# Kernel optimization log

Hardware: AMD Instinct MI355X
Metric: run time of the kernel (lower is better)

The kernel has to match this reference:

```python
import math
import jax, jax.numpy as jnp
import numpy as np

D, N, B, L = 1024, 16, 8, 4096
SCALE = math.sqrt(1.0 / float(N))


def setup_inputs() -> dict:
    key = jax.random.key(0)
    ks = jax.random.split(key, 8)
    x = jax.random.normal(ks[0], (B, D, L), dtype=jnp.float32)
    p_logit = 0.2 * jax.random.normal(ks[1], (D, N), dtype=jnp.float32)
    # reset_parameters(): radius = 1 - sigmoid(p_logit) * delta, phases evenly spaced
    delta = jax.nn.sigmoid(0.2 * jax.random.normal(ks[2], (D, N), dtype=jnp.float32))
    freqs = jnp.exp(jnp.arange(1, D + 1, dtype=jnp.float32) * (-math.log(D) / float(D)))
    freqs = jax.random.permutation(ks[3], freqs)[:, None]            # (D,1)
    theta = freqs * (2.0 * math.pi / float(N))
    phi = theta * jnp.arange(1, N + 1, dtype=jnp.float32)[None, :]   # (D,N)
    p = jax.nn.sigmoid(p_logit)
    radius = 1.0 - p * delta                                         # in (0,1)
    log_q_real = jnp.log(radius)
    log_q_imag = phi
    gamma_real = jax.random.normal(ks[4], (D, N), dtype=jnp.float32)
    gamma_imag = jnp.zeros((D, N), dtype=jnp.float32)
    omega = 0.25 * jax.random.truncated_normal(ks[5], -4.0, 4.0, (D,), dtype=jnp.float32)
    return {"x": x, "p_logit": p_logit, "log_q_real": log_q_real,
            "log_q_imag": log_q_imag, "gamma_real": gamma_real,
            "gamma_imag": gamma_imag, "omega": omega}


def reference(x, p_logit, log_q_real, log_q_imag, gamma_real, gamma_imag, omega):
    # FFT path (hx=None, compute_last_state=False)
    p = jax.nn.sigmoid(p_logit).astype(jnp.float32)                  # (D,N)
    log_q = jax.lax.complex(log_q_real, log_q_imag)                  # complex64 (D,N)
    gamma = jax.lax.complex(gamma_real, gamma_imag) * SCALE          # (D,N)
    t = jnp.arange(L, dtype=jnp.float32)
    # q^t = exp(t * log_q)  (== cumprod of q in the torch code)
    q_pows = jnp.exp(log_q[:, :, None] * t[None, None, :])           # (D,N,L) complex64
    kernel = jnp.einsum('dn,dnl->dl', gamma * p.astype(gamma.dtype), q_pows)  # (D,L)
    fft_len = 1 << int(2 * L - 1).bit_length()
    X = jnp.fft.fft(x.astype(jnp.complex64), n=fft_len, axis=-1)     # (B,D,F)
    K = jnp.fft.fft(kernel, n=fft_len, axis=-1)                      # (D,F)
    y = jnp.fft.ifft(X * K[None], axis=-1)[..., :L].real.astype(x.dtype)
    residual = x * omega[None, :, None]
    return y + residual
```

## Files before the change

kernel.cpp:

```cpp
#include <hip/hip_runtime.h>
#include <hip/hip_bf16.h>
#include <math.h>

#define D_DIM   1024
#define NM      16
#define B_DIM   8
#define L_DIM   4096
#define SCALE_F 0.25f
#define NK      5
#define NITER   8
#define SROW    8704

typedef __attribute__((ext_vector_type(8))) short bf16x8;
typedef __attribute__((ext_vector_type(4))) float f32x4;

union U4 { uint4 u; bf16x8 v; };

__device__ __forceinline__ unsigned short f2bf(float f) {
    __hip_bfloat16 h = __float2bfloat16(f);
    return *reinterpret_cast<unsigned short*>(&h);
}
__device__ __forceinline__ float bflo(unsigned u) { return __uint_as_float(u << 16); }
__device__ __forceinline__ float bfhi(unsigned u) { return __uint_as_float(u & 0xffff0000u); }
__device__ __forceinline__ int swz(int a) { return a ^ (((a >> 7) & 7) << 4); }

__device__ void compute_af_k(int d, int lane, int k,
                             const float* __restrict__ p_logit,
                             const float* __restrict__ lqr,
                             const float* __restrict__ lqi,
                             const float* __restrict__ gr,
                             const float* __restrict__ gi,
                             char* __restrict__ afb)
{
    const int i = lane & 15, g = lane >> 4;
    const int t0 = i - 15 + 32 * k + 8 * g;
    const float t0f = (float)t0;

    float acc[8];
#pragma unroll
    for (int e = 0; e < 8; ++e) acc[e] = 0.0f;

#pragma unroll 1
    for (int n = 0; n < NM; ++n) {
        const int idx = d * NM + n;
        const float pp = 1.0f / (1.0f + __expf(-p_logit[idx]));
        const float CR = gr[idx] * (SCALE_F * pp);
        const float CI = gi[idx] * (SCALE_F * pp);
        const float LR = lqr[idx], LI = lqi[idx];

        float sq, cq; __sincosf(LI, &sq, &cq);
        const float eq = __expf(LR);
        const float qr = eq * cq, qi = eq * sq;
        float s0, c0; __sincosf(t0f * LI, &s0, &c0);
        const float e0 = __expf(t0f * LR);
        float wr = e0 * c0, wi = e0 * s0;

#pragma unroll
        for (int e = 0; e < 8; ++e) {
            acc[e] = fmaf(CR, wr, fmaf(-CI, wi, acc[e]));
            const float nwr = fmaf(wr, qr, -wi * qi);
            const float nwi = fmaf(wr, qi,  wi * qr);
            wr = nwr; wi = nwi;
        }
    }

    unsigned pk[4];
#pragma unroll
    for (int e = 0; e < 8; ++e) {
        const unsigned b = (t0 + e >= 0) ? (unsigned)f2bf(acc[e]) : 0u;
        if ((e & 1) == 0) pk[e >> 1] = b; else pk[e >> 1] |= b << 16;
    }
    *reinterpret_cast<uint4*>(afb + k * 1024 + lane * 16) =
        make_uint4(pk[0], pk[1], pk[2], pk[3]);
}

__global__ __launch_bounds__(512)
void ema_fused(const float* __restrict__ x,
               const float* __restrict__ p_logit,
               const float* __restrict__ lqr, const float* __restrict__ lqi,
               const float* __restrict__ gr, const float* __restrict__ gi,
               const float* __restrict__ omega,
               float* __restrict__ out)
{
    __shared__ __align__(16) char sstage[2][SROW];
    char* safb = sstage[1];

    const int tid  = threadIdx.x;
    const int w    = tid >> 6;
    const int lane = tid & 63;
    const int d    = blockIdx.x;
    const int j    = lane & 15, g = lane >> 4;

    const size_t rstride = (size_t)D_DIM * L_DIM;
    const float* xrow0 = x   + (size_t)d * L_DIM;
    float*       yrow0 = out + (size_t)d * L_DIM;
    const float  om    = omega[d];

    if (tid < 64) {
        const int buf = tid >> 5, h = tid & 31;
        *reinterpret_cast<uint4*>(sstage[buf] + swz(8192 + h * 16)) =
            make_uint4(0u, 0u, 0u, 0u);
    }

    float4 r[2];
#pragma unroll
    for (int v = 0; v < 2; ++v)
        r[v] = *reinterpret_cast<const float4*>(xrow0 + tid * 8 + 4 * v);

    if (w < NK)
        compute_af_k(d, lane, w, p_logit, lqr, lqi, gr, gi, safb);

    __syncthreads();

    bf16x8 af[NK];
#pragma unroll
    for (int k = 0; k < NK; ++k) {
        U4 u; u.u = *reinterpret_cast<const uint4*>(safb + k * 1024 + lane * 16);
        af[k] = u.v;
    }

#define PACK(dst)                                                              \
    {                                                                          \
        unsigned pk0 = (unsigned)f2bf(r[1].w) | ((unsigned)f2bf(r[1].z) << 16);\
        unsigned pk1 = (unsigned)f2bf(r[1].y) | ((unsigned)f2bf(r[1].x) << 16);\
        unsigned pk2 = (unsigned)f2bf(r[0].w) | ((unsigned)f2bf(r[0].z) << 16);\
        unsigned pk3 = (unsigned)f2bf(r[0].y) | ((unsigned)f2bf(r[0].x) << 16);\
        *reinterpret_cast<uint4*>((dst) + swz(8176 - tid * 16)) =              \
            make_uint4(pk0, pk1, pk2, pk3);                                    \
    }

    PACK(sstage[0]);
#pragma unroll
    for (int v = 0; v < 2; ++v)
        r[v] = *reinterpret_cast<const float4*>(xrow0 + rstride + tid * 8 + 4 * v);

    __syncthreads();

#pragma unroll 1
    for (int i = 0; i < NITER; ++i) {
        if (i < NITER - 1) {
            PACK(sstage[(i + 1) & 1]);
            if (i < NITER - 2) {
#pragma unroll
                for (int v = 0; v < 2; ++v)
                    r[v] = *reinterpret_cast<const float4*>(
                        xrow0 + (size_t)(i + 2) * rstride + tid * 8 + 4 * v);
            }
        }

        const char* sb = sstage[i & 1];
        float* yb = yrow0 + (size_t)i * rstride;
#pragma unroll
        for (int tt = 0; tt < 2; ++tt) {
            const int T = 2 * w + tt;
            f32x4 acc = {0.0f, 0.0f, 0.0f, 0.0f};
#pragma unroll
            for (int k = 0; k < NK; ++k) {
                const int rboff = 8160 - 512 * T - 32 * j + 64 * k + 16 * g;
                U4 z; z.u = *reinterpret_cast<const uint4*>(sb + swz(rboff));
                acc = __builtin_amdgcn_mfma_f32_16x16x32_bf16(af[k], z.v, acc, 0, 0, 0);
            }
            const int roff = 8184 - 512 * T - 32 * j - 8 * g;
            const uint2 z2 = *reinterpret_cast<const uint2*>(sb + swz(roff));
            acc.x = fmaf(om, bfhi(z2.y), acc.x);
            acc.y = fmaf(om, bflo(z2.y), acc.y);
            acc.z = fmaf(om, bfhi(z2.x), acc.z);
            acc.w = fmaf(om, bflo(z2.x), acc.w);
            __builtin_nontemporal_store(acc,
                reinterpret_cast<f32x4*>(yb + T * 256 + 16 * j + 4 * g));
        }

        if (i < NITER - 1)
            __syncthreads();
    }
#undef PACK
}

extern "C" void kernel_launch(void* const* d_in, const int* in_sizes, int n_in,
                              void* d_out, int out_size, void* d_ws, size_t ws_size,
                              hipStream_t stream)
{
    const float* x   = (const float*)d_in[0];
    const float* pl  = (const float*)d_in[1];
    const float* lqr = (const float*)d_in[2];
    const float* lqi = (const float*)d_in[3];
    const float* gr  = (const float*)d_in[4];
    const float* gi  = (const float*)d_in[5];
    const float* om  = (const float*)d_in[6];
    float* out = (float*)d_out;

    dim3 grid(D_DIM), block(512);
    ema_fused<<<grid, block, 0, stream>>>(x, pl, lqr, lqi, gr, gi, om, out);
}
```

Before: 48.83 us.

## Give each wave a private LDS window with halo to drop block barriers

Each wave now stages its own 512-sample slice plus a 256-sample causal halo (loaded again from global) into a private double-buffered LDS window, instead of the whole block sharing one row buffer. This removes the per-iteration __syncthreads, and the pre-loop barrier after the first pack, because waves no longer read data written by other waves. The cost is extra global loads for the overlapping halo and more LDS in total.

Result: no change. 48.94 us (+0.2%).

```diff
diff --git a/kernel.cpp b/kernel.cpp
--- a/kernel.cpp
+++ b/kernel.cpp
@@ -9,7 +9,7 @@
 #define SCALE_F 0.25f
 #define NK      5
 #define NITER   8
-#define SROW    8704
+#define WBUF    1536
 
 typedef __attribute__((ext_vector_type(8))) short bf16x8;
 typedef __attribute__((ext_vector_type(4))) float f32x4;
@@ -82,8 +82,8 @@
                const float* __restrict__ omega,
                float* __restrict__ out)
 {
-    __shared__ __align__(16) char sstage[2][SROW];
-    char* safb = sstage[1];
+    __shared__ __align__(16) char swin[8][2][WBUF];
+    __shared__ __align__(16) char safb[NK * 1024];
 
     const int tid  = threadIdx.x;
     const int w    = tid >> 6;
@@ -92,20 +92,17 @@
     const int j    = lane & 15, g = lane >> 4;
 
     const size_t rstride = (size_t)D_DIM * L_DIM;
-    const float* xrow0 = x   + (size_t)d * L_DIM;
-    float*       yrow0 = out + (size_t)d * L_DIM;
-    const float  om    = omega[d];
+    const float* xw = x   + (size_t)d * L_DIM + w * 512;
+    float*       yw = out + (size_t)d * L_DIM + w * 512;
+    const float  om = omega[d];
 
-    if (tid < 64) {
-        const int buf = tid >> 5, h = tid & 31;
-        *reinterpret_cast<uint4*>(sstage[buf] + swz(8192 + h * 16)) =
-            make_uint4(0u, 0u, 0u, 0u);
-    }
-
+    float4 c4 = make_float4(0.f, 0.f, 0.f, 0.f);
+    if (w != 0)
+        c4 = *reinterpret_cast<const float4*>(xw - 256 + lane * 4);
     float4 r[2];
 #pragma unroll
     for (int v = 0; v < 2; ++v)
-        r[v] = *reinterpret_cast<const float4*>(xrow0 + tid * 8 + 4 * v);
+        r[v] = *reinterpret_cast<const float4*>(xw + lane * 8 + 4 * v);
 
     if (w < NK)
         compute_af_k(d, lane, w, p_logit, lqr, lqi, gr, gi, safb);
@@ -121,57 +118,61 @@
 
 #define PACK(dst)                                                              \
     {                                                                          \
+        uint2 cpk = make_uint2(0u, 0u);                                        \
+        if (w != 0) {                                                          \
+            cpk.x = (unsigned)f2bf(c4.w) | ((unsigned)f2bf(c4.z) << 16);       \
+            cpk.y = (unsigned)f2bf(c4.y) | ((unsigned)f2bf(c4.x) << 16);       \
+        }                                                                      \
+        *reinterpret_cast<uint2*>((dst) + swz(1528 - lane * 8)) = cpk;         \
         unsigned pk0 = (unsigned)f2bf(r[1].w) | ((unsigned)f2bf(r[1].z) << 16);\
         unsigned pk1 = (unsigned)f2bf(r[1].y) | ((unsigned)f2bf(r[1].x) << 16);\
         unsigned pk2 = (unsigned)f2bf(r[0].w) | ((unsigned)f2bf(r[0].z) << 16);\
         unsigned pk3 = (unsigned)f2bf(r[0].y) | ((unsigned)f2bf(r[0].x) << 16);\
-        *reinterpret_cast<uint4*>((dst) + swz(8176 - tid * 16)) =              \
+        *reinterpret_cast<uint4*>((dst) + swz(1008 - lane * 16)) =             \
             make_uint4(pk0, pk1, pk2, pk3);                                    \
     }
 
-    PACK(sstage[0]);
+    PACK(&swin[w][0][0]);
+    if (w != 0)
+        c4 = *reinterpret_cast<const float4*>(xw + rstride - 256 + lane * 4);
 #pragma unroll
     for (int v = 0; v < 2; ++v)
-        r[v] = *reinterpret_cast<const float4*>(xrow0 + rstride + tid * 8 + 4 * v);
-
-    __syncthreads();
+        r[v] = *reinterpret_cast<const float4*>(xw + rstride + lane * 8 + 4 * v);
 
 #pragma unroll 1
     for (int i = 0; i < NITER; ++i) {
         if (i < NITER - 1) {
-            PACK(sstage[(i + 1) & 1]);
+            PACK(&swin[w][(i + 1) & 1][0]);
             if (i < NITER - 2) {
+                const float* xn = xw + (size_t)(i + 2) * rstride;
+                if (w != 0)
+                    c4 = *reinterpret_cast<const float4*>(xn - 256 + lane * 4);
 #pragma unroll
                 for (int v = 0; v < 2; ++v)
-                    r[v] = *reinterpret_cast<const float4*>(
-                        xrow0 + (size_t)(i + 2) * rstride + tid * 8 + 4 * v);
+                    r[v] = *reinterpret_cast<const float4*>(xn + lane * 8 + 4 * v);
             }
         }
 
-        const char* sb = sstage[i & 1];
-        float* yb = yrow0 + (size_t)i * rstride;
+        const char* sb = &swin[w][i & 1][0];
+        float* yb = yw + (size_t)i * rstride;
 #pragma unroll
         for (int tt = 0; tt < 2; ++tt) {
-            const int T = 2 * w + tt;
             f32x4 acc = {0.0f, 0.0f, 0.0f, 0.0f};
 #pragma unroll
             for (int k = 0; k < NK; ++k) {
-                const int rboff = 8160 - 512 * T - 32 * j + 64 * k + 16 * g;
+                const int rboff = 992 - 512 * tt - 32 * j + 64 * k + 16 * g;
                 U4 z; z.u = *reinterpret_cast<const uint4*>(sb + swz(rboff));
                 acc = __builtin_amdgcn_mfma_f32_16x16x32_bf16(af[k], z.v, acc, 0, 0, 0);
             }
-            const int roff = 8184 - 512 * T - 32 * j - 8 * g;
+            const int roff = 1016 - 512 * tt - 32 * j - 8 * g;
             const uint2 z2 = *reinterpret_cast<const uint2*>(sb + swz(roff));
             acc.x = fmaf(om, bfhi(z2.y), acc.x);
             acc.y = fmaf(om, bflo(z2.y), acc.y);
             acc.z = fmaf(om, bfhi(z2.x), acc.z);
             acc.w = fmaf(om, bflo(z2.x), acc.w);
             __builtin_nontemporal_store(acc,
-                reinterpret_cast<f32x4*>(yb + T * 256 + 16 * j + 4 * g));
+                reinterpret_cast<f32x4*>(yb + tt * 256 + 16 * j + 4 * g));
         }
-
-        if (i < NITER - 1)
-            __syncthreads();
     }
 #undef PACK
 }
```
